# Performance work log

Measured on AMD Instinct MI355X. Metric: run time of the kernel, lower is better.

## Reference

```python
import jax, jax.numpy as jnp
import numpy as np

HID = 2048   # hidden_size
H = 16       # num_attention_heads
KV = 2       # num_key_value_heads
HD = 256     # head_dim
S = 2048     # seq_len (prefill)
MAX_SEQ = 4096
EPS = 1e-6
RD = HD // 4          # partial RoPE dims (head_dim * 0.25)
SCALE = HD ** (-0.5)
GROUPS = H // KV


def setup_inputs() -> dict:
    key = jax.random.key(0)
    ks = jax.random.split(key, 10)
    hidden_in = jax.random.normal(ks[0], (1, S, HID), jnp.float32)
    ang = jax.random.uniform(ks[1], (1, S, RD), jnp.float32) * (2.0 * np.pi)
    cos = jnp.cos(ang)
    sin = jnp.sin(ang)
    w = 0.02
    q_proj_w = jax.random.normal(ks[2], (2 * H * HD, HID), jnp.float32) * w
    k_proj_w = jax.random.normal(ks[3], (KV * HD, HID), jnp.float32) * w
    v_proj_w = jax.random.normal(ks[4], (KV * HD, HID), jnp.float32) * w
    o_proj_w = jax.random.normal(ks[5], (HID, H * HD), jnp.float32) * w
    q_norm_w = jax.random.normal(ks[6], (HD,), jnp.float32) * 0.1
    k_norm_w = jax.random.normal(ks[7], (HD,), jnp.float32) * 0.1
    return dict(hidden_in=hidden_in, cos=cos, sin=sin,
                q_proj_w=q_proj_w, k_proj_w=k_proj_w, v_proj_w=v_proj_w,
                o_proj_w=o_proj_w, q_norm_w=q_norm_w, k_norm_w=k_norm_w)


def _rmsnorm(x, w):
    var = jnp.mean(x * x, axis=-1, keepdims=True)
    return x * jax.lax.rsqrt(var + EPS) * (1.0 + w)


def _rotate_half(x):
    x1, x2 = jnp.split(x, 2, axis=-1)
    return jnp.concatenate([-x2, x1], axis=-1)


def reference(hidden_in, cos, sin, q_proj_w, k_proj_w, v_proj_w, o_proj_w, q_norm_w, k_norm_w):
    # projections (F.linear => x @ W^T)
    qg = hidden_in @ q_proj_w.T                      # [1, S, 2*H*HD]
    k = hidden_in @ k_proj_w.T                       # [1, S, KV*HD]
    v = hidden_in @ v_proj_w.T

    qg = qg.reshape(1, S, H, 2 * HD)
    q, gate = qg[..., :HD], qg[..., HD:]             # chunk(2, dim=-1)
    gate = gate.reshape(1, S, H * HD)

    q = _rmsnorm(q, q_norm_w).transpose(0, 2, 1, 3)  # [1, H, S, HD]
    k = _rmsnorm(k.reshape(1, S, KV, HD), k_norm_w).transpose(0, 2, 1, 3)  # [1, KV, S, HD]
    v = v.reshape(1, S, KV, HD).transpose(0, 2, 1, 3)                      # [1, KV, S, HD]

    # partial RoPE on first RD dims
    c = cos[:, None, :, :]                           # [1, 1, S, RD]
    s = sin[:, None, :, :]
    q_rot, q_pass = q[..., :RD], q[..., RD:]
    k_rot, k_pass = k[..., :RD], k[..., RD:]
    q = jnp.concatenate([q_rot * c + _rotate_half(q_rot) * s, q_pass], axis=-1)
    k = jnp.concatenate([k_rot * c + _rotate_half(k_rot) * s, k_pass], axis=-1)

    # KV cache padded to max_seq
    zpad = jnp.zeros((1, KV, MAX_SEQ - S, HD), k.dtype)
    k_cache_out = jnp.concatenate([k, zpad], axis=2)
    v_cache_out = jnp.concatenate([v, zpad], axis=2)

    # GQA repeat
    k_r = jnp.repeat(k, GROUPS, axis=1)              # [1, H, S, HD]
    v_r = jnp.repeat(v, GROUPS, axis=1)

    causal = jnp.triu(jnp.full((S, S), -10000.0, jnp.float32), k=1)
    scores = jnp.einsum('bhqd,bhkd->bhqk', q, k_r) * SCALE + causal
    attn_w = jax.nn.softmax(scores, axis=-1)
    attn = jnp.einsum('bhqk,bhkd->bhqd', attn_w, v_r)
    attn = attn.transpose(0, 2, 1, 3).reshape(1, S, H * HD)

    attn = attn * jax.nn.sigmoid(gate)
    hidden_out = attn @ o_proj_w.T                   # [1, S, HID]
    return hidden_out, k_cache_out, v_cache_out
```

## Files before the change

### kernel.cpp

```cpp
#include <hip/hip_runtime.h>

#define S_LEN 2048
#define HID 2048
#define NH 16
#define NKV 2
#define HD 256
#define MAXSEQ 4096
#define NALL 9216
#define RD 64

typedef __attribute__((ext_vector_type(8))) short short8_t;
typedef __attribute__((ext_vector_type(4))) float float4_t;

#define DPPF(x, ctrl) __builtin_bit_cast(float, __builtin_amdgcn_update_dpp( \
    __builtin_bit_cast(int, x), __builtin_bit_cast(int, x), ctrl, 0xF, 0xF, false))

__device__ __forceinline__ unsigned short f2b(float f) {
  union { float f; unsigned u; } v; v.f = f;
  unsigned u = v.u;
  return (unsigned short)((u + 0x7FFFu + ((u >> 16) & 1u)) >> 16);
}

__device__ __forceinline__ void gload_lds16(const void* g, void* l) {
  __builtin_amdgcn_global_load_lds(
      (const __attribute__((address_space(1))) void*)g,
      (__attribute__((address_space(3))) void*)l, 16, 0, 0);
}

__global__ void fused_cvt(const float* __restrict__ hidden, const float* __restrict__ qw,
                          const float* __restrict__ kw, const float* __restrict__ vw,
                          const float* __restrict__ ow,
                          unsigned short* __restrict__ hidb, unsigned short* __restrict__ wallb,
                          unsigned short* __restrict__ wob,
                          float* __restrict__ kcache, float* __restrict__ vcache) {
  const long i = (long)blockIdx.x * 256 + threadIdx.x;
  const long N0 = 1048576, N1 = N0 + 4194304, N2 = N1 + 262144, N3 = N2 + 262144,
             N4 = N3 + 2097152;
  if (i < N4) {
    const float* s; unsigned short* d; long j;
    if (i < N0)      { s = hidden; d = hidb;  j = i; }
    else if (i < N1) { s = qw; d = wallb;                        j = i - N0; }
    else if (i < N2) { s = kw; d = wallb + (size_t)8192*HID;     j = i - N1; }
    else if (i < N3) { s = vw; d = wallb + (size_t)8704*HID;     j = i - N2; }
    else             { s = ow; d = wob;                          j = i - N3; }
    float4 v = ((const float4*)s)[j];
    short4 o;
    o.x = (short)f2b(v.x); o.y = (short)f2b(v.y);
    o.z = (short)f2b(v.z); o.w = (short)f2b(v.w);
    ((short4*)d)[j] = o;
  } else {
    long j = i - N4;
    int region = (int)(j >> 17);
    long o = j & 131071;
    float* base = (region < 2 ? kcache : vcache)
                + (size_t)(region & 1) * MAXSEQ * HD + (size_t)S_LEN * HD;
    float4 z; z.x = 0.f; z.y = 0.f; z.z = 0.f; z.w = 0.f;
    ((float4*)base)[o] = z;
  }
}

template<int BM, int BN, int MI, int NI>
__global__ __launch_bounds__(256, 2) void gemm_bt(
    const unsigned short* __restrict__ A, const unsigned short* __restrict__ B,
    float* __restrict__ C, int M, int N, int K) {
  constexpr int BK = 64;
  __shared__ unsigned short As[BM * BK];
  __shared__ unsigned short Bs[BN * BK];
  const int tid = threadIdx.x;
  const int lane = tid & 63;
  const int w = tid >> 6;
  const int wr = w >> 1, wc = w & 1;
  const int l15 = lane & 15, l4 = lane >> 4;
  const int M0 = blockIdx.y * BM, N0 = blockIdx.x * BN;
  float4_t acc[MI][NI] = {};
  for (int kt = 0; kt < K; kt += BK) {
    __syncthreads();
#pragma unroll
    for (int i = 0; i < BM/32; ++i) {
      int c = tid + i*256;
      int row = c >> 3;
      gload_lds16(A + (size_t)(M0 + row)*K + kt + ((c & 7) ^ (row & 7))*8, (char*)As + c*16);
    }
#pragma unroll
    for (int i = 0; i < BN/32; ++i) {
      int c = tid + i*256;
      int row = c >> 3;
      gload_lds16(B + (size_t)(N0 + row)*K + kt + ((c & 7) ^ (row & 7))*8, (char*)Bs + c*16);
    }
    __syncthreads();
#pragma unroll
    for (int ks = 0; ks < 2; ++ks) {
      short8_t af[MI], bf[NI];
#pragma unroll
      for (int mi = 0; mi < MI; ++mi) {
        int row = wr*(BM/2) + mi*16 + l15;
        af[mi] = *(const short8_t*)&As[row*BK + ((ks*4 + l4) ^ (l15 & 7))*8];
      }
#pragma unroll
      for (int ni = 0; ni < NI; ++ni) {
        int row = wc*(BN/2) + ni*16 + l15;
        bf[ni] = *(const short8_t*)&Bs[row*BK + ((ks*4 + l4) ^ (l15 & 7))*8];
      }
#pragma unroll
      for (int mi = 0; mi < MI; ++mi)
#pragma unroll
        for (int ni = 0; ni < NI; ++ni)
          acc[mi][ni] = __builtin_amdgcn_mfma_f32_16x16x32_bf16(af[mi], bf[ni], acc[mi][ni], 0, 0, 0);
    }
  }
#pragma unroll
  for (int mi = 0; mi < MI; ++mi) {
    int rb = M0 + wr*(BM/2) + mi*16 + l4*4;
#pragma unroll
    for (int ni = 0; ni < NI; ++ni) {
      int col = N0 + wc*(BN/2) + ni*16 + l15;
#pragma unroll
      for (int r = 0; r < 4; ++r)
        C[(size_t)(rb + r)*N + col] = acc[mi][ni][r];
    }
  }
}

__global__ void postproc(const float* __restrict__ C1,
                         const float* __restrict__ cosb, const float* __restrict__ sinb,
                         const float* __restrict__ qnw, const float* __restrict__ knw,
                         unsigned short* __restrict__ qb, unsigned short* __restrict__ kb,
                         unsigned short* __restrict__ vtb,
                         float* __restrict__ kcache, float* __restrict__ vcache) {
  const int w = threadIdx.x >> 6, lane = threadIdx.x & 63;
  const int s = blockIdx.x*4 + w;
  const int t = blockIdx.y;
  const int d = lane*4;
  const float* rowp;
  if (t < 16)      rowp = C1 + (size_t)s*NALL + t*512;
  else if (t < 18) rowp = C1 + (size_t)s*NALL + 8192 + (t-16)*256;
  else             rowp = C1 + (size_t)s*NALL + 8704 + (t-18)*256;
  float4 x = *(const float4*)(rowp + d);
  if (t >= 18) {
    int kvi = t - 18;
    *(float4*)(vcache + (size_t)kvi*MAXSEQ*HD + (size_t)s*HD + d) = x;
    unsigned short* vt = vtb + (size_t)kvi*HD*S_LEN;
    vt[(size_t)(d+0)*S_LEN + s] = f2b(x.x);
    vt[(size_t)(d+1)*S_LEN + s] = f2b(x.y);
    vt[(size_t)(d+2)*S_LEN + s] = f2b(x.z);
    vt[(size_t)(d+3)*S_LEN + s] = f2b(x.w);
    return;
  }
  float ss = x.x*x.x + x.y*x.y + x.z*x.z + x.w*x.w;
#pragma unroll
  for (int o = 32; o >= 1; o >>= 1) ss += __shfl_xor(ss, o, 64);
  float rn = rsqrtf(ss*(1.0f/256.0f) + 1e-6f);
  const float* nw = (t < 16) ? qnw : knw;
  float4 g = *(const float4*)(nw + d);
  float4 y;
  y.x = x.x*rn*(1.f+g.x); y.y = x.y*rn*(1.f+g.y);
  y.z = x.z*rn*(1.f+g.z); y.w = x.w*rn*(1.f+g.w);
  float px = __shfl_xor(y.x, 8, 64);
  float py = __shfl_xor(y.y, 8, 64);
  float pz = __shfl_xor(y.z, 8, 64);
  float pw = __shfl_xor(y.w, 8, 64);
  if (lane < 16) {
    float sgn = (lane & 8) ? 1.f : -1.f;
    float4 cs = *(const float4*)(cosb + (size_t)s*RD + d);
    float4 sn = *(const float4*)(sinb + (size_t)s*RD + d);
    y.x = y.x*cs.x + sgn*px*sn.x;
    y.y = y.y*cs.y + sgn*py*sn.y;
    y.z = y.z*cs.z + sgn*pz*sn.z;
    y.w = y.w*cs.w + sgn*pw*sn.w;
  }
  if (t < 16) {
    const float qs = 0.0625f * 1.44269504088896f;
    short4 o;
    o.x = (short)f2b(y.x*qs); o.y = (short)f2b(y.y*qs);
    o.z = (short)f2b(y.z*qs); o.w = (short)f2b(y.w*qs);
    *(short4*)(qb + (size_t)t*S_LEN*HD + (size_t)s*HD + d) = o;
  } else {
    int kvi = t - 16;
    *(float4*)(kcache + (size_t)kvi*MAXSEQ*HD + (size_t)s*HD + d) = y;
    short4 o;
    o.x = (short)f2b(y.x); o.y = (short)f2b(y.y);
    o.z = (short)f2b(y.z); o.w = (short)f2b(y.w);
    *(short4*)(kb + (size_t)kvi*S_LEN*HD + (size_t)s*HD + d) = o;
  }
}

__global__ __launch_bounds__(256, 2) void attn_kernel(
    const unsigned short* __restrict__ qb, const unsigned short* __restrict__ kb,
    const unsigned short* __restrict__ vtb, const float* __restrict__ C1,
    unsigned short* __restrict__ attnb) {
  __shared__ char smem[36864];
  unsigned short* Ks  = (unsigned short*)smem;
  unsigned short* VTs = (unsigned short*)(smem + 16384);
  const int tid = threadIdx.x, lane = tid & 63, w = tid >> 6;
  const int l15 = lane & 15, l4 = lane >> 4;
  const int b = blockIdx.x;
  const int i2 = b >> 1;
  const int h = i2 & 15;
  const int t16 = i2 >> 4;
  const int qt = (b & 1) ? (31 - t16) : t16;
  const int kv = h >> 3;
  const int q0 = qt * 64;
  const unsigned short* Qb = qb + (size_t)h*S_LEN*HD;
  const unsigned short* Kb = kb + (size_t)kv*S_LEN*HD;
  const unsigned short* Vb = vtb + (size_t)kv*HD*S_LEN;
  unsigned short* Pw = (unsigned short*)(smem + 32768 + w*1024);
  const int qrow = q0 + w*16 + l15;
  short8_t qf[8];
#pragma unroll
  for (int kk = 0; kk < 8; ++kk)
    qf[kk] = *(const short8_t*)(Qb + (size_t)qrow*HD + kk*32 + l4*8);
  float4_t oacc[16] = {};
  float m_run[4] = {-1e30f, -1e30f, -1e30f, -1e30f};
  float l_run[4] = {0.f, 0.f, 0.f, 0.f};
  const int nIter = 2*qt + 2;
  for (int kbI = 0; kbI < nIter; ++kbI) {
    const int k0 = kbI * 32;
    __syncthreads();
#pragma unroll
    for (int i = 0; i < 4; ++i) {
      int c = tid + i*256;
      int row = c >> 5;
      gload_lds16(Kb + (size_t)(k0 + row)*HD + ((c & 31) ^ (row & 7))*8, (char*)Ks + c*16);
    }
#pragma unroll
    for (int i = 0; i < 4; ++i) {
      int c = tid + i*256;
      int row = c >> 2;
      gload_lds16(Vb + (size_t)row*S_LEN + k0 + ((c & 3) ^ ((row >> 1) & 3))*8, (char*)VTs + c*16);
    }
    __syncthreads();
    float4_t sacc[2] = {};
#pragma unroll
    for (int nt = 0; nt < 2; ++nt)
#pragma unroll
      for (int kk = 0; kk < 8; ++kk) {
        short8_t bfr = *(const short8_t*)&Ks[(nt*16 + l15)*HD + ((kk*4 + l4) ^ (l15 & 7))*8];
        sacc[nt] = __builtin_amdgcn_mfma_f32_16x16x32_bf16(qf[kk], bfr, sacc[nt], 0, 0, 0);
      }
    if (kbI >= 2*qt) {
#pragma unroll
      for (int nt = 0; nt < 2; ++nt)
#pragma unroll
        for (int r = 0; r < 4; ++r)
          if (k0 + nt*16 + l15 > q0 + w*16 + l4*4 + r) sacc[nt][r] = -1e30f;
    }
    float alpha[4], p[2][4];
#pragma unroll
    for (int r = 0; r < 4; ++r) {
      float m0 = fmaxf(sacc[0][r], sacc[1][r]);
      m0 = fmaxf(m0, DPPF(m0, 0xB1));
      m0 = fmaxf(m0, DPPF(m0, 0x4E));
      m0 = fmaxf(m0, DPPF(m0, 0x141));
      m0 = fmaxf(m0, DPPF(m0, 0x140));
      float mnew = fmaxf(m_run[r], m0);
      alpha[r] = exp2f(m_run[r] - mnew);
      m_run[r] = mnew;
      float sum = 0.f;
#pragma unroll
      for (int nt = 0; nt < 2; ++nt) {
        p[nt][r] = exp2f(sacc[nt][r] - mnew);
        sum += p[nt][r];
      }
      sum += DPPF(sum, 0xB1);
      sum += DPPF(sum, 0x4E);
      sum += DPPF(sum, 0x141);
      sum += DPPF(sum, 0x140);
      l_run[r] = l_run[r]*alpha[r] + sum;
    }
#pragma unroll
    for (int nt2 = 0; nt2 < 16; ++nt2) {
      oacc[nt2][0] *= alpha[0];
      oacc[nt2][1] *= alpha[1];
      oacc[nt2][2] *= alpha[2];
      oacc[nt2][3] *= alpha[3];
    }
#pragma unroll
    for (int nt = 0; nt < 2; ++nt)
#pragma unroll
      for (int r = 0; r < 4; ++r) {
        int prow = l4*4 + r;
        int pcol = nt*16 + l15;
        Pw[prow*32 + (((pcol >> 3) ^ ((prow >> 1) & 3)))*8 + (pcol & 7)] = f2b(p[nt][r]);
      }
    short8_t pf = *(const short8_t*)&Pw[l15*32 + ((l4 ^ ((l15 >> 1) & 3)))*8];
#pragma unroll
    for (int nt2 = 0; nt2 < 16; ++nt2) {
      int vrow = nt2*16 + l15;
      short8_t v0 = *(const short8_t*)&VTs[vrow*32 + ((l4 ^ ((vrow >> 1) & 3)))*8];
      oacc[nt2] = __builtin_amdgcn_mfma_f32_16x16x32_bf16(pf, v0, oacc[nt2], 0, 0, 0);
    }
  }
  float inv_l[4];
#pragma unroll
  for (int r = 0; r < 4; ++r) inv_l[r] = 1.f / l_run[r];
  const int srow0 = q0 + w*16 + l4*4;
#pragma unroll
  for (int nt2 = 0; nt2 < 16; ++nt2) {
    int dim = nt2*16 + l15;
#pragma unroll
    for (int r = 0; r < 4; ++r) {
      int srow = srow0 + r;
      float gv = C1[(size_t)srow*NALL + h*512 + 256 + dim];
      float sg = 1.f / (1.f + __expf(-gv));
      attnb[(size_t)srow*(NH*HD) + h*HD + dim] = f2b(oacc[nt2][r] * inv_l[r] * sg);
    }
  }
}

extern "C" void kernel_launch(void* const* d_in, const int* in_sizes, int n_in,
                              void* d_out, int out_size, void* d_ws, size_t ws_size,
                              hipStream_t stream) {
  const float* hidden = (const float*)d_in[0];
  const float* cosb   = (const float*)d_in[1];
  const float* sinb   = (const float*)d_in[2];
  const float* qw     = (const float*)d_in[3];
  const float* kw     = (const float*)d_in[4];
  const float* vw     = (const float*)d_in[5];
  const float* ow     = (const float*)d_in[6];
  const float* qnw    = (const float*)d_in[7];
  const float* knw    = (const float*)d_in[8];
  float* out    = (float*)d_out;
  float* kcache = out + (size_t)S_LEN*HID;
  float* vcache = kcache + (size_t)NKV*MAXSEQ*HD;

  char* ws = (char*)d_ws;
  size_t off = 0;
  auto alloc = [&](size_t bytes) -> char* {
    char* p = ws + off; off += (bytes + 255) & ~(size_t)255; return p;
  };
  unsigned short* hidb  = (unsigned short*)alloc((size_t)S_LEN*HID*2);
  unsigned short* wallb = (unsigned short*)alloc((size_t)NALL*HID*2);
  unsigned short* wob   = (unsigned short*)alloc((size_t)HID*NH*HD*2);
  float*          C1    = (float*)alloc((size_t)S_LEN*NALL*4);
  unsigned short* qb    = (unsigned short*)alloc((size_t)NH*S_LEN*HD*2);
  unsigned short* kb    = (unsigned short*)alloc((size_t)NKV*S_LEN*HD*2);
  unsigned short* vtb   = (unsigned short*)alloc((size_t)NKV*HD*S_LEN*2);
  unsigned short* attnb = (unsigned short*)alloc((size_t)S_LEN*NH*HD*2);

  fused_cvt<<<32768, 256, 0, stream>>>(hidden, qw, kw, vw, ow,
                                       hidb, wallb, wob, kcache, vcache);

  gemm_bt<128,128,4,4><<<dim3(NALL/128, S_LEN/128), 256, 0, stream>>>(
      hidb, wallb, C1, S_LEN, NALL, HID);

  postproc<<<dim3(S_LEN/4, 20), 256, 0, stream>>>(
      C1, cosb, sinb, qnw, knw, qb, kb, vtb, kcache, vcache);

  attn_kernel<<<512, 256, 0, stream>>>(qb, kb, vtb, C1, attnb);

  gemm_bt<128,128,4,4><<<dim3(HID/128, S_LEN/128), 256, 0, stream>>>(
      attnb, wob, out, S_LEN, HID, NH*HD);
}
```

Baseline: 483.3 us.

## Split attention KV range across two wave groups and skip redundant softmax rescales

Each attention block now runs 512 threads as two groups of four waves. Each group handles half of the key/value tiles for the same 64 query rows, with its own K/V LDS buffers. The two partial softmax states are merged through LDS at the end. The online-softmax rescale of the output accumulators is also skipped unless the running max grows by more than a threshold, which cuts per-tile ALU work. The cost is doubled LDS use, an extra merge pass with barriers, and lower occupancy per block.

```diff
diff --git a/kernel.cpp b/kernel.cpp
--- a/kernel.cpp
+++ b/kernel.cpp
@@ -184,15 +184,19 @@
   }
 }
 
-__global__ __launch_bounds__(256, 2) void attn_kernel(
+__global__ __launch_bounds__(512, 4) void attn_kernel(
     const unsigned short* __restrict__ qb, const unsigned short* __restrict__ kb,
     const unsigned short* __restrict__ vtb, const float* __restrict__ C1,
     unsigned short* __restrict__ attnb) {
-  __shared__ char smem[36864];
-  unsigned short* Ks  = (unsigned short*)smem;
-  unsigned short* VTs = (unsigned short*)(smem + 16384);
+  __shared__ char smem[73728];
   const int tid = threadIdx.x, lane = tid & 63, w = tid >> 6;
+  const int g  = w >> 2;
+  const int wq = w & 3;
+  const int gtid = tid & 255;
   const int l15 = lane & 15, l4 = lane >> 4;
+  unsigned short* Ks  = (unsigned short*)(smem + g*16384);
+  unsigned short* VTs = (unsigned short*)(smem + 32768 + g*16384);
+  unsigned short* Pw  = (unsigned short*)(smem + 65536 + w*1024);
   const int b = blockIdx.x;
   const int i2 = b >> 1;
   const int h = i2 & 15;
@@ -203,8 +207,7 @@
   const unsigned short* Qb = qb + (size_t)h*S_LEN*HD;
   const unsigned short* Kb = kb + (size_t)kv*S_LEN*HD;
   const unsigned short* Vb = vtb + (size_t)kv*HD*S_LEN;
-  unsigned short* Pw = (unsigned short*)(smem + 32768 + w*1024);
-  const int qrow = q0 + w*16 + l15;
+  const int qrow = q0 + wq*16 + l15;
   short8_t qf[8];
 #pragma unroll
   for (int kk = 0; kk < 8; ++kk)
@@ -212,19 +215,21 @@
   float4_t oacc[16] = {};
   float m_run[4] = {-1e30f, -1e30f, -1e30f, -1e30f};
   float l_run[4] = {0.f, 0.f, 0.f, 0.f};
-  const int nIter = 2*qt + 2;
-  for (int kbI = 0; kbI < nIter; ++kbI) {
-    const int k0 = kbI * 32;
+  const int nIt = qt + 1;
+  const int tbase = g * nIt;
+  for (int it = 0; it < nIt; ++it) {
+    const int tIdx = tbase + it;
+    const int k0 = tIdx * 32;
     __syncthreads();
 #pragma unroll
     for (int i = 0; i < 4; ++i) {
-      int c = tid + i*256;
+      int c = gtid + i*256;
       int row = c >> 5;
       gload_lds16(Kb + (size_t)(k0 + row)*HD + ((c & 31) ^ (row & 7))*8, (char*)Ks + c*16);
     }
 #pragma unroll
     for (int i = 0; i < 4; ++i) {
-      int c = tid + i*256;
+      int c = gtid + i*256;
       int row = c >> 2;
       gload_lds16(Vb + (size_t)row*S_LEN + k0 + ((c & 3) ^ ((row >> 1) & 3))*8, (char*)VTs + c*16);
     }
@@ -237,42 +242,52 @@
         short8_t bfr = *(const short8_t*)&Ks[(nt*16 + l15)*HD + ((kk*4 + l4) ^ (l15 & 7))*8];
         sacc[nt] = __builtin_amdgcn_mfma_f32_16x16x32_bf16(qf[kk], bfr, sacc[nt], 0, 0, 0);
       }
-    if (kbI >= 2*qt) {
+    if (tIdx >= 2*qt) {
 #pragma unroll
       for (int nt = 0; nt < 2; ++nt)
 #pragma unroll
         for (int r = 0; r < 4; ++r)
-          if (k0 + nt*16 + l15 > q0 + w*16 + l4*4 + r) sacc[nt][r] = -1e30f;
-    }
-    float alpha[4], p[2][4];
+          if (k0 + nt*16 + l15 > q0 + wq*16 + l4*4 + r) sacc[nt][r] = -1e30f;
+    }
+    float m0[4], p[2][4];
 #pragma unroll
     for (int r = 0; r < 4; ++r) {
-      float m0 = fmaxf(sacc[0][r], sacc[1][r]);
-      m0 = fmaxf(m0, DPPF(m0, 0xB1));
-      m0 = fmaxf(m0, DPPF(m0, 0x4E));
-      m0 = fmaxf(m0, DPPF(m0, 0x141));
-      m0 = fmaxf(m0, DPPF(m0, 0x140));
-      float mnew = fmaxf(m_run[r], m0);
-      alpha[r] = exp2f(m_run[r] - mnew);
-      m_run[r] = mnew;
-      float sum = 0.f;
-#pragma unroll
-      for (int nt = 0; nt < 2; ++nt) {
-        p[nt][r] = exp2f(sacc[nt][r] - mnew);
-        sum += p[nt][r];
-      }
+      float v = fmaxf(sacc[0][r], sacc[1][r]);
+      v = fmaxf(v, DPPF(v, 0xB1));
+      v = fmaxf(v, DPPF(v, 0x4E));
+      v = fmaxf(v, DPPF(v, 0x141));
+      v = fmaxf(v, DPPF(v, 0x140));
+      m0[r] = v;
+    }
+    int need = (m0[0] > m_run[0] + 4.f) | (m0[1] > m_run[1] + 4.f) |
+               (m0[2] > m_run[2] + 4.f) | (m0[3] > m_run[3] + 4.f);
+    if (__any(need)) {
+      float al[4];
+#pragma unroll
+      for (int r = 0; r < 4; ++r) {
+        float mnew = fmaxf(m_run[r], m0[r]);
+        al[r] = exp2f(m_run[r] - mnew);
+        m_run[r] = mnew;
+        l_run[r] *= al[r];
+      }
+#pragma unroll
+      for (int nt2 = 0; nt2 < 16; ++nt2) {
+        oacc[nt2][0] *= al[0];
+        oacc[nt2][1] *= al[1];
+        oacc[nt2][2] *= al[2];
+        oacc[nt2][3] *= al[3];
+      }
+    }
+#pragma unroll
+    for (int r = 0; r < 4; ++r) {
+      p[0][r] = exp2f(sacc[0][r] - m_run[r]);
+      p[1][r] = exp2f(sacc[1][r] - m_run[r]);
+      float sum = p[0][r] + p[1][r];
       sum += DPPF(sum, 0xB1);
       sum += DPPF(sum, 0x4E);
       sum += DPPF(sum, 0x141);
       sum += DPPF(sum, 0x140);
-      l_run[r] = l_run[r]*alpha[r] + sum;
-    }
-#pragma unroll
-    for (int nt2 = 0; nt2 < 16; ++nt2) {
-      oacc[nt2][0] *= alpha[0];
-      oacc[nt2][1] *= alpha[1];
-      oacc[nt2][2] *= alpha[2];
-      oacc[nt2][3] *= alpha[3];
+      l_run[r] += sum;
     }
 #pragma unroll
     for (int nt = 0; nt < 2; ++nt)
@@ -290,19 +305,46 @@
       oacc[nt2] = __builtin_amdgcn_mfma_f32_16x16x32_bf16(pf, v0, oacc[nt2], 0, 0, 0);
     }
   }
-  float inv_l[4];
-#pragma unroll
-  for (int r = 0; r < 4; ++r) inv_l[r] = 1.f / l_run[r];
-  const int srow0 = q0 + w*16 + l4*4;
-#pragma unroll
-  for (int nt2 = 0; nt2 < 16; ++nt2) {
-    int dim = nt2*16 + l15;
+  __syncthreads();
+  float* Od = (float*)smem;
+  float* ML = (float*)(smem + 69632);
+  const int r0 = wq*16 + l4*4;
+  if (g == 1) {
+#pragma unroll
+    for (int r = 0; r < 4; ++r)
+      if (l15 == 0) { ML[(r0 + r)*2] = m_run[r]; ML[(r0 + r)*2 + 1] = l_run[r]; }
+#pragma unroll
+    for (int nt2 = 0; nt2 < 16; ++nt2) {
+      int dim = nt2*16 + l15;
+#pragma unroll
+      for (int r = 0; r < 4; ++r)
+        Od[(r0 + r)*258 + dim] = oacc[nt2][r];
+    }
+  }
+  __syncthreads();
+  if (g == 0) {
+    float fA[4], fB[4], inv_l[4];
 #pragma unroll
     for (int r = 0; r < 4; ++r) {
-      int srow = srow0 + r;
-      float gv = C1[(size_t)srow*NALL + h*512 + 256 + dim];
-      float sg = 1.f / (1.f + __expf(-gv));
-      attnb[(size_t)srow*(NH*HD) + h*HD + dim] = f2b(oacc[nt2][r] * inv_l[r] * sg);
+      float mB = ML[(r0 + r)*2];
+      float lB = ML[(r0 + r)*2 + 1];
+      float m = fmaxf(m_run[r], mB);
+      fA[r] = exp2f(m_run[r] - m);
+      fB[r] = exp2f(mB - m);
+      inv_l[r] = 1.f / (l_run[r]*fA[r] + lB*fB[r]);
+    }
+    const int srow0 = q0 + wq*16 + l4*4;
+#pragma unroll
+    for (int nt2 = 0; nt2 < 16; ++nt2) {
+      int dim = nt2*16 + l15;
+#pragma unroll
+      for (int r = 0; r < 4; ++r) {
+        int srow = srow0 + r;
+        float ov = oacc[nt2][r]*fA[r] + Od[(r0 + r)*258 + dim]*fB[r];
+        float gv = C1[(size_t)srow*NALL + h*512 + 256 + dim];
+        float sg = 1.f / (1.f + __expf(-gv));
+        attnb[(size_t)srow*(NH*HD) + h*HD + dim] = f2b(ov * inv_l[r] * sg);
+      }
     }
   }
 }
@@ -346,7 +388,7 @@
   postproc<<<dim3(S_LEN/4, 20), 256, 0, stream>>>(
       C1, cosb, sinb, qnw, knw, qb, kb, vtb, kcache, vcache);
 
-  attn_kernel<<<512, 256, 0, stream>>>(qb, kb, vtb, C1, attnb);
+  attn_kernel<<<512, 512, 0, stream>>>(qb, kb, vtb, C1, attnb);
 
   gemm_bt<128,128,4,4><<<dim3(HID/128, S_LEN/128), 256, 0, stream>>>(
       attnb, wob, out, S_LEN, HID, NH*HD);
```

Result: slower. 687.5 us (+42.2%).

## Double-buffer K/V tiles in attention and skip rescale when max barely grows

Applied to the files above, without the earlier changes.

The attention loop now prefetches the next K/V tile into a second LDS buffer while the current one is computed, using explicit vmcnt waits and raw barriers instead of two syncthreads per iteration. Separately, it adds a lazy-rescale online softmax: the running max and the output accumulators are only updated when some row's block max exceeds the running max by more than a threshold. This is meant to hide global-to-LDS latency and cut per-iteration VALU rescaling work. The cost is LDS growing from 36KB to 68KB, which may reduce occupancy, and skipped rescales can let exp2 values exceed 1, which raises overflow and precision risk.

```diff
diff --git a/kernel.cpp b/kernel.cpp
--- a/kernel.cpp
+++ b/kernel.cpp
@@ -188,9 +188,7 @@
     const unsigned short* __restrict__ qb, const unsigned short* __restrict__ kb,
     const unsigned short* __restrict__ vtb, const float* __restrict__ C1,
     unsigned short* __restrict__ attnb) {
-  __shared__ char smem[36864];
-  unsigned short* Ks  = (unsigned short*)smem;
-  unsigned short* VTs = (unsigned short*)(smem + 16384);
+  __shared__ char smem[69632];
   const int tid = threadIdx.x, lane = tid & 63, w = tid >> 6;
   const int l15 = lane & 15, l4 = lane >> 4;
   const int b = blockIdx.x;
@@ -203,7 +201,7 @@
   const unsigned short* Qb = qb + (size_t)h*S_LEN*HD;
   const unsigned short* Kb = kb + (size_t)kv*S_LEN*HD;
   const unsigned short* Vb = vtb + (size_t)kv*HD*S_LEN;
-  unsigned short* Pw = (unsigned short*)(smem + 32768 + w*1024);
+  unsigned short* Pw = (unsigned short*)(smem + 65536 + w*1024);
   const int qrow = q0 + w*16 + l15;
   short8_t qf[8];
 #pragma unroll
@@ -213,22 +211,39 @@
   float m_run[4] = {-1e30f, -1e30f, -1e30f, -1e30f};
   float l_run[4] = {0.f, 0.f, 0.f, 0.f};
   const int nIter = 2*qt + 2;
-  for (int kbI = 0; kbI < nIter; ++kbI) {
-    const int k0 = kbI * 32;
-    __syncthreads();
+
+  auto STAGE = [&](int tI, int buf) {
+    const int k0s = tI * 32;
+    char* KsD = smem + buf*16384;
+    char* VTD = smem + 32768 + buf*16384;
 #pragma unroll
     for (int i = 0; i < 4; ++i) {
       int c = tid + i*256;
       int row = c >> 5;
-      gload_lds16(Kb + (size_t)(k0 + row)*HD + ((c & 31) ^ (row & 7))*8, (char*)Ks + c*16);
+      gload_lds16(Kb + (size_t)(k0s + row)*HD + ((c & 31) ^ (row & 7))*8, KsD + c*16);
     }
 #pragma unroll
     for (int i = 0; i < 4; ++i) {
       int c = tid + i*256;
       int row = c >> 2;
-      gload_lds16(Vb + (size_t)row*S_LEN + k0 + ((c & 3) ^ ((row >> 1) & 3))*8, (char*)VTs + c*16);
-    }
-    __syncthreads();
+      gload_lds16(Vb + (size_t)row*S_LEN + k0s + ((c & 3) ^ ((row >> 1) & 3))*8, VTD + c*16);
+    }
+  };
+
+  STAGE(0, 0);
+  for (int kbI = 0; kbI < nIter; ++kbI) {
+    const int cur = kbI & 1;
+    if (kbI + 1 < nIter) {
+      STAGE(kbI + 1, cur ^ 1);
+      asm volatile("s_waitcnt vmcnt(8)" ::: "memory");
+    } else {
+      asm volatile("s_waitcnt vmcnt(0)" ::: "memory");
+    }
+    __builtin_amdgcn_s_barrier();
+    asm volatile("" ::: "memory");
+    const unsigned short* Ks  = (const unsigned short*)(smem + cur*16384);
+    const unsigned short* VTs = (const unsigned short*)(smem + 32768 + cur*16384);
+    const int k0 = kbI * 32;
     float4_t sacc[2] = {};
 #pragma unroll
     for (int nt = 0; nt < 2; ++nt)
@@ -244,35 +259,45 @@
         for (int r = 0; r < 4; ++r)
           if (k0 + nt*16 + l15 > q0 + w*16 + l4*4 + r) sacc[nt][r] = -1e30f;
     }
-    float alpha[4], p[2][4];
+    float m0[4], p[2][4];
 #pragma unroll
     for (int r = 0; r < 4; ++r) {
-      float m0 = fmaxf(sacc[0][r], sacc[1][r]);
-      m0 = fmaxf(m0, DPPF(m0, 0xB1));
-      m0 = fmaxf(m0, DPPF(m0, 0x4E));
-      m0 = fmaxf(m0, DPPF(m0, 0x141));
-      m0 = fmaxf(m0, DPPF(m0, 0x140));
-      float mnew = fmaxf(m_run[r], m0);
-      alpha[r] = exp2f(m_run[r] - mnew);
-      m_run[r] = mnew;
-      float sum = 0.f;
-#pragma unroll
-      for (int nt = 0; nt < 2; ++nt) {
-        p[nt][r] = exp2f(sacc[nt][r] - mnew);
-        sum += p[nt][r];
-      }
+      float v = fmaxf(sacc[0][r], sacc[1][r]);
+      v = fmaxf(v, DPPF(v, 0xB1));
+      v = fmaxf(v, DPPF(v, 0x4E));
+      v = fmaxf(v, DPPF(v, 0x141));
+      v = fmaxf(v, DPPF(v, 0x140));
+      m0[r] = v;
+    }
+    int need = (m0[0] > m_run[0] + 4.f) | (m0[1] > m_run[1] + 4.f) |
+               (m0[2] > m_run[2] + 4.f) | (m0[3] > m_run[3] + 4.f);
+    if (__any(need)) {
+      float al[4];
+#pragma unroll
+      for (int r = 0; r < 4; ++r) {
+        float mnew = fmaxf(m_run[r], m0[r]);
+        al[r] = exp2f(m_run[r] - mnew);
+        m_run[r] = mnew;
+        l_run[r] *= al[r];
+      }
+#pragma unroll
+      for (int nt2 = 0; nt2 < 16; ++nt2) {
+        oacc[nt2][0] *= al[0];
+        oacc[nt2][1] *= al[1];
+        oacc[nt2][2] *= al[2];
+        oacc[nt2][3] *= al[3];
+      }
+    }
+#pragma unroll
+    for (int r = 0; r < 4; ++r) {
+      p[0][r] = exp2f(sacc[0][r] - m_run[r]);
+      p[1][r] = exp2f(sacc[1][r] - m_run[r]);
+      float sum = p[0][r] + p[1][r];
       sum += DPPF(sum, 0xB1);
       sum += DPPF(sum, 0x4E);
       sum += DPPF(sum, 0x141);
       sum += DPPF(sum, 0x140);
-      l_run[r] = l_run[r]*alpha[r] + sum;
-    }
-#pragma unroll
-    for (int nt2 = 0; nt2 < 16; ++nt2) {
-      oacc[nt2][0] *= alpha[0];
-      oacc[nt2][1] *= alpha[1];
-      oacc[nt2][2] *= alpha[2];
-      oacc[nt2][3] *= alpha[3];
+      l_run[r] += sum;
     }
 #pragma unroll
     for (int nt = 0; nt < 2; ++nt)
@@ -289,6 +314,8 @@
       short8_t v0 = *(const short8_t*)&VTs[vrow*32 + ((l4 ^ ((vrow >> 1) & 3)))*8];
       oacc[nt2] = __builtin_amdgcn_mfma_f32_16x16x32_bf16(pf, v0, oacc[nt2], 0, 0, 0);
     }
+    asm volatile("" ::: "memory");
+    __builtin_amdgcn_s_barrier();
   }
   float inv_l[4];
 #pragma unroll
```

Result: faster. 449.9 us (-6.9%).
